# Optimization experiments

Hardware: AMD Instinct MI355X
Metric: run time of the kernel (lower is better)

Reference implementation:

```python
import jax, jax.numpy as jnp
import numpy as np

VOCAB = 40000
EMB = 128
INNER = 128
Q_LEN = 20


def setup_inputs() -> dict:
    key = jax.random.key(0)
    ks = jax.random.split(key, 16)
    B, S, NB = 32, 512, 20
    std = 0.1
    inp = {
        "memories": jax.random.normal(ks[0], (B, S, NB, EMB), jnp.float32),
        "stories": jax.random.normal(ks[1], (B, S, EMB), jnp.float32),
        "stories_mask": jnp.ones((B, S), jnp.float32),
        "queries": jax.random.randint(ks[2], (B, Q_LEN), 0, VOCAB, jnp.int32),
        "keys": jax.random.randint(ks[3], (NB,), 0, VOCAB, jnp.int32),
        # learned parameters
        "emb_table": jax.random.normal(ks[4], (VOCAB, EMB), jnp.float32) * std,
        "mult_mask": jnp.ones((Q_LEN, EMB), jnp.float32),
        "A": jax.random.normal(ks[5], (EMB, INNER), jnp.float32) * std,
        "Bm": jax.random.normal(ks[6], (EMB, INNER), jnp.float32) * std,
        "C": jax.random.normal(ks[7], (EMB, INNER), jnp.float32) * std,
        "v": jnp.ones((INNER,), jnp.float32),
        "D": jax.random.normal(ks[8], (EMB, INNER), jnp.float32) * std,
        "E": jax.random.normal(ks[9], (EMB, INNER), jnp.float32) * std,
        "F": jax.random.normal(ks[10], (EMB, INNER), jnp.float32) * std,
        "w": jnp.ones((INNER,), jnp.float32),
        "H": jax.random.normal(ks[11], (EMB, EMB), jnp.float32) * std,
        "R": jax.random.normal(ks[12], (EMB, VOCAB), jnp.float32) * std,
    }
    return inp


def reference(memories, stories, stories_mask, queries, keys,
              emb_table, mult_mask, A, Bm, C, v, D, E, F, w, H, R):
    # _reduce_query: embed tokens, apply positional multiplicative mask, sum over positions
    u = jnp.sum(emb_table[queries] * mult_mask, axis=1)            # [B, emb]

    # intratemporal (Bahdanau-style) attention over memory blocks
    ia = jnp.einsum('bsne,ei->bsni', memories, A)                  # [B,S,NB,inner]
    kb = emb_table[keys] @ Bm                                      # [NB,inner]
    qc = u @ C                                                     # [B,inner]
    intr_align = jnp.sum(v * jnp.tanh(ia + kb[None, None] + qc[:, None, None]), axis=3)  # [B,S,NB]
    intr_attn = jax.nn.softmax(intr_align, axis=2)[..., None]      # [B,S,NB,1]
    temporal_memory = jnp.sum(intr_attn * memories, axis=2)        # [B,S,emb]

    # temporal attention over story sentences (with sentence term E, softmax activation)
    td = temporal_memory @ D                                       # [B,S,inner]
    te = stories @ E                                               # [B,S,inner]
    tf = (u @ F)[:, None]                                          # [B,1,inner]
    temporal_align_unmasked = jnp.sum(w * jnp.tanh(td + te + tf), axis=2)  # [B,S]
    temporal_align = temporal_align_unmasked * stories_mask
    # softmax branch: additive -inf mask where stories_mask == 0 (inf*0 NaNs zeroed in torch)
    masked_logits = jnp.where(stories_mask != 0, temporal_align, -jnp.inf)
    temporal_attn = jax.nn.softmax(masked_logits, axis=1)          # [B,S]

    # output readout (standard memory-network head)
    o = jnp.sum(temporal_attn[..., None] * temporal_memory, axis=1)  # [B,emb]
    logits = (o + u @ H) @ R                                         # [B,vocab]
    return logits
```

## Files before the change

### kernel.cpp

```cpp
#include <hip/hip_runtime.h>
#include <hip/hip_bf16.h>

#define B_   32
#define S_   512
#define NB_  20
#define EMB_ 128
#define VOC_ 40000

typedef float f32x4 __attribute__((ext_vector_type(4)));
typedef _Float16 f16x8 __attribute__((ext_vector_type(8)));
typedef __fp16 fp16x2 __attribute__((ext_vector_type(2)));

union FragH { uint4 u; f16x8 h; };
union H2 { fp16x2 h; unsigned u; };

__device__ __forceinline__ unsigned pk2(float a, float b){
  H2 t; t.h = __builtin_amdgcn_cvt_pkrtz(a, b);
  return t.u;
}
__device__ __forceinline__ unsigned short f2h(float x){
  _Float16 h = (_Float16)x;
  return __builtin_bit_cast(unsigned short, h);
}
__device__ __forceinline__ float tanh_fast(float x){
  float e2 = __builtin_amdgcn_exp2f(x * 2.8853900817779268f);
  float r  = __builtin_amdgcn_rcpf(e2 + 1.f);
  return fmaf(-2.f, r, 1.f);
}


__global__ __launch_bounds__(128) void prep_kernel(
    const int* __restrict__ queries, const int* __restrict__ keys,
    const float* __restrict__ emb, const float* __restrict__ mmask,
    const float* __restrict__ A, const float* __restrict__ Bm,
    const float* __restrict__ C, const float* __restrict__ D,
    const float* __restrict__ E, const float* __restrict__ F,
    const float* __restrict__ H,
    float* __restrict__ tf_w, float* __restrict__ uh_w,
    float* __restrict__ kbq_w,
    unsigned short* __restrict__ afrag, unsigned short* __restrict__ w2frag)
{
  int bid = blockIdx.x, tid = threadIdx.x;
  if (bid < 32) {
    __shared__ float ulds[128];
    int b = bid;
    float s = 0.f;
    for (int q=0;q<NB_;q++){
      int tok = queries[b*NB_+q];
      s += emb[tok*128+tid]*mmask[q*128+tid];
    }
    ulds[tid] = s;
    __syncthreads();
    float sf=0.f, sh=0.f;
    for (int e=0;e<128;e++){
      float uv = ulds[e];
      sf += uv*F[e*128+tid];
      sh += uv*H[e*128+tid];
    }
    tf_w[b*128+tid]=sf; uh_w[b*128+tid]=sh;
  } else if (bid < 672) {
    __shared__ float ulds[128];
    __shared__ float ek[128];
    int idx = bid-32;
    int b = idx/20, n = idx - b*20;
    float s = 0.f;
    for (int q=0;q<NB_;q++){
      int tok = queries[b*NB_+q];
      s += emb[tok*128+tid]*mmask[q*128+tid];
    }
    ulds[tid] = s;
    ek[tid] = emb[keys[n]*128+tid];
    __syncthreads();
    float acc = 0.f;
    for (int e=0;e<128;e++){
      acc += ulds[e]*C[e*128+tid] + ek[e]*Bm[e*128+tid];
    }
    kbq_w[idx*128+tid] = acc;
  } else if (bid < 680) {
    int a = bid-672;
    for (int cc=0;cc<2;cc++){
      int c = (a*128+tid)*2+cc;
      int lane = c&63, kc = (c>>6)&3, nt = c>>8;
      int n2 = nt*16 + (lane&15);
      int k0 = kc*32 + (lane>>4)*8;
      alignas(16) unsigned short t[8];
      #pragma unroll
      for (int j=0;j<8;j++) t[j] = f2h(A[(k0+j)*128+n2]);
      *(uint4*)(afrag + c*8) = *(const uint4*)t;
    }
  } else {
    int wb = bid-680;
    for (int cc=0;cc<2;cc++){
      int c = (wb*128+tid)*2+cc;
      int lane = c&63, kc = (c>>6)&7, nt = c>>9;
      int n2 = nt*16 + (lane&15);
      int k0 = kc*32 + (lane>>4)*8;
      alignas(16) unsigned short t[8];
      #pragma unroll
      for (int j=0;j<8;j++){
        int k = k0+j;
        float x = (k<128) ? D[k*128+n2] : E[(k-128)*128+n2];
        t[j] = f2h(x);
      }
      *(uint4*)(w2frag + c*8) = *(const uint4*)t;
    }
  }
}

__global__ __launch_bounds__(256) void k2_kernel(
    const float* __restrict__ mem, const unsigned short* __restrict__ afrag,
    const float* __restrict__ kbq_w, const float* __restrict__ vvec,
    const float* __restrict__ stories, const unsigned short* __restrict__ w2frag,
    const float* __restrict__ tf_w, const float* __restrict__ wvec,
    const float* __restrict__ smask,
    unsigned short* __restrict__ tm_h, float* __restrict__ talign_w)
{
  __shared__ unsigned short mfr[5*4*64*8];
  __shared__ float alignP[4*80];
  __shared__ float attns[80];
  __shared__ float partial2[16];

  int g = blockIdx.x, tid = threadIdx.x;
  int b = g >> 7;

  int w = tid>>6, lane = tid&63;
  int lo16 = lane & 15, hi16 = lane >> 4;
  int p2 = w, e0 = (tid&63)*2;

  float2 sto = *(const float2*)(stories + ((size_t)(g*4+p2))*128 + e0);

  {
    int kq = (tid&31)*4;
    int kgs = kq>>5, s2s = (kq>>3)&3, offs = kq&7;
    int r0 = tid>>5;
    int cbs = s2s ^ ((kgs&1)<<2);
    int slot_e = (s2s<<4) | ((r0 ^ cbs) & 15);
    int slot_o = (s2s<<4) | (((r0^8) ^ cbs) & 15);
    unsigned addr_e = (unsigned)((kgs*64 + slot_e)*16 + offs*2);
    unsigned addr_o = (unsigned)((kgs*64 + slot_o)*16 + offs*2);
    const float4* gm = (const float4*)(mem) + (size_t)g*2560 + tid;
    #pragma unroll
    for (int mt=0; mt<5; ++mt){
      float4 d0 = gm[(2*mt)*256];
      float4 d1 = gm[(2*mt+1)*256];
      *(uint2*)((char*)mfr + addr_e + mt*4096) = make_uint2(pk2(d0.x,d0.y), pk2(d0.z,d0.w));
      *(uint2*)((char*)mfr + addr_o + mt*4096) = make_uint2(pk2(d1.x,d1.y), pk2(d1.z,d1.w));
    }
  }
  __syncthreads();

  int i0 = w*32 + lo16, i1 = i0 + 16;
  float vv0 = vvec[i0],       vv1 = vvec[i1];
  float tf0 = tf_w[b*128+i0], tf1 = tf_w[b*128+i1];
  float wv0 = wvec[i0],       wv1 = wvec[i1];
  const float* kbq0 = kbq_w + b*(NB_*128) + i0;

  f32x4 acc[5][2];
  #pragma unroll
  for (int mt=0;mt<5;mt++){ acc[mt][0]=(f32x4)(0.f); acc[mt][1]=(f32x4)(0.f); }
  #pragma unroll
  for (int kc=0;kc<4;kc++){
    FragH b0, b1;
    b0.u = *(const uint4*)(afrag + ((size_t)((2*w)*4+kc)*64 + lane)*8);
    b1.u = *(const uint4*)(afrag + ((size_t)((2*w+1)*4+kc)*64 + lane)*8);
    int slot = (hi16<<4) | ((lo16 ^ hi16 ^ ((kc&1)<<2)) & 15);
    #pragma unroll
    for (int mt=0;mt<5;mt++){
      FragH a;
      a.u = *(const uint4*)(mfr + ((mt*4+kc)*64 + slot)*8);
      acc[mt][0] = __builtin_amdgcn_mfma_f32_16x16x32_f16(a.h, b0.h, acc[mt][0], 0,0,0);
      acc[mt][1] = __builtin_amdgcn_mfma_f32_16x16x32_f16(a.h, b1.h, acc[mt][1], 0,0,0);
    }
  }

  #pragma unroll
  for (int mt=0;mt<5;mt++){
    #pragma unroll
    for (int r=0;r<4;r++){
      unsigned row = mt*16 + hi16*4 + r;
      unsigned p = row/20u;
      unsigned n = row - p*20u;
      float z0 = acc[mt][0][r] + kbq0[n*128];
      float z1 = acc[mt][1][r] + kbq0[n*128+16];
      float part = vv0*tanh_fast(z0) + vv1*tanh_fast(z1);
      part += __shfl_xor(part, 1);
      part += __shfl_xor(part, 2);
      part += __shfl_xor(part, 4);
      part += __shfl_xor(part, 8);
      if (lo16 == 0) alignP[w*80+row] = part;
    }
  }
  __syncthreads();

  {
    float av = -1e30f;
    if (lane < 20){
      int idx = w*20 + lane;
      av = alignP[idx] + alignP[80+idx] + alignP[160+idx] + alignP[240+idx];
    }
    float mx = av;
    #pragma unroll
    for (int d=1; d<64; d<<=1) mx = fmaxf(mx, __shfl_xor(mx, d));
    float ev = (lane<20) ? __expf(av - mx) : 0.f;
    float sm = ev;
    #pragma unroll
    for (int d=1; d<64; d<<=1) sm += __shfl_xor(sm, d);
    if (lane<20) attns[w*20+lane] = ev * __builtin_amdgcn_rcpf(sm);
  }

  unsigned otm;
  {
    int kg = e0>>5, s2 = (e0>>3)&3;
    int cb = s2 ^ ((kg&1)<<2);
    unsigned base = (unsigned)((kg*64 + (s2<<4))*16 + (e0&7)*2);
    float2 o = make_float2(0.f,0.f);
    #define TM_STEP(ROW) { \
      H2 q; q.u = *(const unsigned*)((const char*)mfr + base + (((ROW)>>4)*4096) + ((((ROW)&15) ^ cb) & 15)*16); \
      float a = attns[(ROW)]; \
      o.x += a*(float)q.h[0]; \
      o.y += a*(float)q.h[1]; }
    #define TM_20(P) { \
      TM_STEP((P)*20+0)  TM_STEP((P)*20+1)  TM_STEP((P)*20+2)  TM_STEP((P)*20+3)  \
      TM_STEP((P)*20+4)  TM_STEP((P)*20+5)  TM_STEP((P)*20+6)  TM_STEP((P)*20+7)  \
      TM_STEP((P)*20+8)  TM_STEP((P)*20+9)  TM_STEP((P)*20+10) TM_STEP((P)*20+11) \
      TM_STEP((P)*20+12) TM_STEP((P)*20+13) TM_STEP((P)*20+14) TM_STEP((P)*20+15) \
      TM_STEP((P)*20+16) TM_STEP((P)*20+17) TM_STEP((P)*20+18) TM_STEP((P)*20+19) }
    switch(p2){
      case 0: TM_20(0) break;
      case 1: TM_20(1) break;
      case 2: TM_20(2) break;
      default: TM_20(3) break;
    }
    #undef TM_20
    #undef TM_STEP
    otm = pk2(o.x, o.y);
    *(unsigned*)(tm_h + ((size_t)g*4+p2)*128 + e0) = otm;
  }
  __syncthreads();

  {
    int kcA = e0>>5;
    int lane2 = (((e0>>3)&3)<<4) | p2;
    *(unsigned*)(mfr + (kcA*64+lane2)*8 + (e0&7)) = otm;
    *(unsigned*)(mfr + ((kcA+4)*64+lane2)*8 + (e0&7)) = pk2(sto.x, sto.y);
  }
  __syncthreads();

  {
    f32x4 acc0 = (f32x4)(0.f), acc1 = (f32x4)(0.f);
    #pragma unroll
    for (int kc=0;kc<8;kc++){
      FragH af, b0, b1;
      af.u = *(const uint4*)(mfr + (kc*64+lane)*8);
      b0.u = *(const uint4*)(w2frag + ((size_t)((2*w)*8+kc)*64+lane)*8);
      b1.u = *(const uint4*)(w2frag + ((size_t)((2*w+1)*8+kc)*64+lane)*8);
      acc0 = __builtin_amdgcn_mfma_f32_16x16x32_f16(af.h, b0.h, acc0, 0,0,0);
      acc1 = __builtin_amdgcn_mfma_f32_16x16x32_f16(af.h, b1.h, acc1, 0,0,0);
    }
    if (hi16 == 0){
      #pragma unroll
      for (int r=0;r<4;r++){
        float part = wv0*tanh_fast(acc0[r] + tf0) + wv1*tanh_fast(acc1[r] + tf1);
        part += __shfl_xor(part,1);
        part += __shfl_xor(part,2);
        part += __shfl_xor(part,4);
        part += __shfl_xor(part,8);
        if (lo16==0) partial2[w*4+r] = part;
      }
    }
  }
  __syncthreads();

  if (tid < 4){
    float ta = partial2[tid]+partial2[4+tid]+partial2[8+tid]+partial2[12+tid];
    int flat = g*4+tid;
    float m = smask[flat];
    talign_w[flat] = (m != 0.0f) ? ta*m : -INFINITY;
  }
}

__global__ __launch_bounds__(256) void k3_kernel(
    const float* __restrict__ talign_w, const unsigned short* __restrict__ tm_h,
    const float* __restrict__ uh_w, float* __restrict__ ov_w)
{
  __shared__ float attn[512];
  __shared__ float red[256];
  __shared__ float2 red2[256];
  int bid = blockIdx.x, tid = threadIdx.x;
  int b = bid >> 3, ec = bid & 7;

  float v0 = talign_w[b*512+tid];
  float v1 = talign_w[b*512+256+tid];
  red[tid] = fmaxf(v0,v1);
  __syncthreads();
  for (int s=128;s>0;s>>=1){ if (tid<s) red[tid]=fmaxf(red[tid],red[tid+s]); __syncthreads(); }
  float M = red[0];
  __syncthreads();
  float e0v = __expf(v0-M), e1v = __expf(v1-M);
  red[tid] = e0v+e1v;
  __syncthreads();
  for (int s=128;s>0;s>>=1){ if (tid<s) red[tid]+=red[tid+s]; __syncthreads(); }
  float invZ = 1.f/red[0];
  attn[tid] = e0v*invZ;
  attn[256+tid] = e1v*invZ;
  __syncthreads();

  int e = ec*16 + (tid&7)*2;
  int sg = tid>>3;
  const unsigned short* tmb = tm_h + ((size_t)b*512 + sg*16)*128 + e;
  float2 a2 = make_float2(0.f,0.f);
  #pragma unroll 8
  for (int i=0;i<16;i++){
    H2 q; q.u = *(const unsigned*)(tmb + (size_t)i*128);
    float at = attn[sg*16+i];
    a2.x += at*(float)q.h[0];
    a2.y += at*(float)q.h[1];
  }
  red2[tid] = a2;
  __syncthreads();
  for (int s=128;s>=8;s>>=1){
    if (tid<s){ red2[tid].x += red2[tid+s].x; red2[tid].y += red2[tid+s].y; }
    __syncthreads();
  }
  if (tid<8){
    int e2 = ec*16 + tid*2;
    ov_w[b*128+e2]   = red2[tid].x + uh_w[b*128+e2];
    ov_w[b*128+e2+1] = red2[tid].y + uh_w[b*128+e2+1];
  }
}

__global__ __launch_bounds__(256) void k4_kernel(
    const float* __restrict__ ov_w, const float* __restrict__ R,
    float* __restrict__ out)
{
  int tid = threadIdx.x;
  int j = blockIdx.x*128 + (tid&63)*2;
  if (j >= VOC_) return;
  int bh = tid>>6;
  const float* ovb = ov_w + bh*8*128;
  float2 acc[8];
  #pragma unroll
  for (int bb=0;bb<8;bb++) acc[bb]=make_float2(0.f,0.f);
  for (int e=0;e<128;e+=4){
    float2 r0 = *(const float2*)(&R[(size_t)(e+0)*VOC_ + j]);
    float2 r1 = *(const float2*)(&R[(size_t)(e+1)*VOC_ + j]);
    float2 r2 = *(const float2*)(&R[(size_t)(e+2)*VOC_ + j]);
    float2 r3 = *(const float2*)(&R[(size_t)(e+3)*VOC_ + j]);
    #pragma unroll
    for (int bb=0;bb<8;bb++){
      float4 o = *(const float4*)(&ovb[bb*128+e]);
      acc[bb].x += o.x*r0.x + o.y*r1.x + o.z*r2.x + o.w*r3.x;
      acc[bb].y += o.x*r0.y + o.y*r1.y + o.z*r2.y + o.w*r3.y;
    }
  }
  #pragma unroll
  for (int bb=0;bb<8;bb++)
    *(float2*)(&out[(size_t)(bh*8+bb)*VOC_ + j]) = acc[bb];
}

extern "C" void kernel_launch(void* const* d_in, const int* in_sizes, int n_in,
                              void* d_out, int out_size, void* d_ws, size_t ws_size,
                              hipStream_t stream)
{
  const float* mem    = (const float*)d_in[0];
  const float* stories= (const float*)d_in[1];
  const float* smask  = (const float*)d_in[2];
  const int*   queries= (const int*)d_in[3];
  const int*   keys   = (const int*)d_in[4];
  const float* emb    = (const float*)d_in[5];
  const float* mmask  = (const float*)d_in[6];
  const float* A      = (const float*)d_in[7];
  const float* Bm     = (const float*)d_in[8];
  const float* C      = (const float*)d_in[9];
  const float* vvec   = (const float*)d_in[10];
  const float* D      = (const float*)d_in[11];
  const float* E      = (const float*)d_in[12];
  const float* F      = (const float*)d_in[13];
  const float* wvec   = (const float*)d_in[14];
  const float* H      = (const float*)d_in[15];
  const float* R      = (const float*)d_in[16];
  float* out = (float*)d_out;

  char* ws = (char*)d_ws;
  float* tf_w             = (float*)(ws + 0);
  float* uh_w             = (float*)(ws + 16384);
  float* kbq_w            = (float*)(ws + 32768);
  unsigned short* afrag   = (unsigned short*)(ws + 360448);
  unsigned short* w2frag  = (unsigned short*)(ws + 393216);
  unsigned short* tm_h    = (unsigned short*)(ws + 458752);
  float* talign_w         = (float*)(ws + 4653056);
  float* ov_w             = (float*)(ws + 4718592);

  prep_kernel<<<696,128,0,stream>>>(queries, keys, emb, mmask, A, Bm, C, D, E, F, H,
                                    tf_w, uh_w, kbq_w, afrag, w2frag);
  k2_kernel<<<4096,256,0,stream>>>(mem, afrag, kbq_w, vvec,
                                   stories, w2frag, tf_w, wvec, smask,
                                   tm_h, talign_w);
  k3_kernel<<<256,256,0,stream>>>(talign_w, tm_h, uh_w, ov_w);
  k4_kernel<<<313,256,0,stream>>>(ov_w, R, out);
}
```

Measured before the change: 370.7 us.

## Halve story positions per k2 block and double the grid

The intratemporal/temporal kernel now handles 2 story positions per 256-thread block instead of 4, and the launch grid doubles to 8192 blocks. Shared-memory staging shrinks to 3 MFMA row tiles, which should let more blocks be resident and spread the memory loads across more workgroups. In exchange, 8 of the 48 MFMA rows are padding, half the threads sit idle in the weighted-sum and store phases, and per-block fixed costs (weight fragment loads, barriers) are paid twice as often.

```diff
diff --git a/kernel.cpp b/kernel.cpp
--- a/kernel.cpp
+++ b/kernel.cpp
@@ -115,19 +115,21 @@
     const float* __restrict__ smask,
     unsigned short* __restrict__ tm_h, float* __restrict__ talign_w)
 {
-  __shared__ unsigned short mfr[5*4*64*8];
-  __shared__ float alignP[4*80];
-  __shared__ float attns[80];
-  __shared__ float partial2[16];
+  __shared__ unsigned short mfr[3*4*64*8];
+  __shared__ float alignP[4*40];
+  __shared__ float attns[40];
+  __shared__ float partial2[8];
 
   int g = blockIdx.x, tid = threadIdx.x;
-  int b = g >> 7;
+  int b = g >> 8;
 
   int w = tid>>6, lane = tid&63;
   int lo16 = lane & 15, hi16 = lane >> 4;
-  int p2 = w, e0 = (tid&63)*2;
-
-  float2 sto = *(const float2*)(stories + ((size_t)(g*4+p2))*128 + e0);
+
+  float2 sto = make_float2(0.f,0.f);
+  int p2s = (tid>>6)&1, e0s = (tid&63)*2;
+  if (tid >= 128)
+    sto = *(const float2*)(stories + ((size_t)(g*2+p2s))*128 + e0s);
 
   {
     int kq = (tid&31)*4;
@@ -138,14 +140,17 @@
     int slot_o = (s2s<<4) | (((r0^8) ^ cbs) & 15);
     unsigned addr_e = (unsigned)((kgs*64 + slot_e)*16 + offs*2);
     unsigned addr_o = (unsigned)((kgs*64 + slot_o)*16 + offs*2);
-    const float4* gm = (const float4*)(mem) + (size_t)g*2560 + tid;
-    #pragma unroll
-    for (int mt=0; mt<5; ++mt){
-      float4 d0 = gm[(2*mt)*256];
-      float4 d1 = gm[(2*mt+1)*256];
-      *(uint2*)((char*)mfr + addr_e + mt*4096) = make_uint2(pk2(d0.x,d0.y), pk2(d0.z,d0.w));
-      *(uint2*)((char*)mfr + addr_o + mt*4096) = make_uint2(pk2(d1.x,d1.y), pk2(d1.z,d1.w));
-    }
+    const float4* gm = (const float4*)(mem) + (size_t)g*1280 + tid;
+    float4 d0 = gm[0];
+    float4 d1 = gm[256];
+    float4 d2 = gm[512];
+    float4 d3 = gm[768];
+    float4 d4 = gm[1024];
+    *(uint2*)((char*)mfr + addr_e)        = make_uint2(pk2(d0.x,d0.y), pk2(d0.z,d0.w));
+    *(uint2*)((char*)mfr + addr_o)        = make_uint2(pk2(d1.x,d1.y), pk2(d1.z,d1.w));
+    *(uint2*)((char*)mfr + addr_e + 4096) = make_uint2(pk2(d2.x,d2.y), pk2(d2.z,d2.w));
+    *(uint2*)((char*)mfr + addr_o + 4096) = make_uint2(pk2(d3.x,d3.y), pk2(d3.z,d3.w));
+    *(uint2*)((char*)mfr + addr_e + 8192) = make_uint2(pk2(d4.x,d4.y), pk2(d4.z,d4.w));
   }
   __syncthreads();
 
@@ -155,9 +160,9 @@
   float wv0 = wvec[i0],       wv1 = wvec[i1];
   const float* kbq0 = kbq_w + b*(NB_*128) + i0;
 
-  f32x4 acc[5][2];
+  f32x4 acc[3][2];
   #pragma unroll
-  for (int mt=0;mt<5;mt++){ acc[mt][0]=(f32x4)(0.f); acc[mt][1]=(f32x4)(0.f); }
+  for (int mt=0;mt<3;mt++){ acc[mt][0]=(f32x4)(0.f); acc[mt][1]=(f32x4)(0.f); }
   #pragma unroll
   for (int kc=0;kc<4;kc++){
     FragH b0, b1;
@@ -165,7 +170,7 @@
     b1.u = *(const uint4*)(afrag + ((size_t)((2*w+1)*4+kc)*64 + lane)*8);
     int slot = (hi16<<4) | ((lo16 ^ hi16 ^ ((kc&1)<<2)) & 15);
     #pragma unroll
-    for (int mt=0;mt<5;mt++){
+    for (int mt=0;mt<3;mt++){
       FragH a;
       a.u = *(const uint4*)(mfr + ((mt*4+kc)*64 + slot)*8);
       acc[mt][0] = __builtin_amdgcn_mfma_f32_16x16x32_f16(a.h, b0.h, acc[mt][0], 0,0,0);
@@ -174,29 +179,31 @@
   }
 
   #pragma unroll
-  for (int mt=0;mt<5;mt++){
+  for (int mt=0;mt<3;mt++){
     #pragma unroll
     for (int r=0;r<4;r++){
       unsigned row = mt*16 + hi16*4 + r;
-      unsigned p = row/20u;
-      unsigned n = row - p*20u;
-      float z0 = acc[mt][0][r] + kbq0[n*128];
-      float z1 = acc[mt][1][r] + kbq0[n*128+16];
-      float part = vv0*tanh_fast(z0) + vv1*tanh_fast(z1);
-      part += __shfl_xor(part, 1);
-      part += __shfl_xor(part, 2);
-      part += __shfl_xor(part, 4);
-      part += __shfl_xor(part, 8);
-      if (lo16 == 0) alignP[w*80+row] = part;
-    }
-  }
-  __syncthreads();
-
-  {
+      if (row < 40){
+        unsigned p = row/20u;
+        unsigned n = row - p*20u;
+        float z0 = acc[mt][0][r] + kbq0[n*128];
+        float z1 = acc[mt][1][r] + kbq0[n*128+16];
+        float part = vv0*tanh_fast(z0) + vv1*tanh_fast(z1);
+        part += __shfl_xor(part, 1);
+        part += __shfl_xor(part, 2);
+        part += __shfl_xor(part, 4);
+        part += __shfl_xor(part, 8);
+        if (lo16 == 0) alignP[w*40+row] = part;
+      }
+    }
+  }
+  __syncthreads();
+
+  if (w < 2){
     float av = -1e30f;
     if (lane < 20){
       int idx = w*20 + lane;
-      av = alignP[idx] + alignP[80+idx] + alignP[160+idx] + alignP[240+idx];
+      av = alignP[idx] + alignP[40+idx] + alignP[80+idx] + alignP[120+idx];
     }
     float mx = av;
     #pragma unroll
@@ -208,11 +215,12 @@
     if (lane<20) attns[w*20+lane] = ev * __builtin_amdgcn_rcpf(sm);
   }
 
-  unsigned otm;
-  {
-    int kg = e0>>5, s2 = (e0>>3)&3;
+  unsigned otm = 0;
+  int p2t = tid>>6, e0t = (tid&63)*2;
+  if (tid < 128){
+    int kg = e0t>>5, s2 = (e0t>>3)&3;
     int cb = s2 ^ ((kg&1)<<2);
-    unsigned base = (unsigned)((kg*64 + (s2<<4))*16 + (e0&7)*2);
+    unsigned base = (unsigned)((kg*64 + (s2<<4))*16 + (e0t&7)*2);
     float2 o = make_float2(0.f,0.f);
     #define TM_STEP(ROW) { \
       H2 q; q.u = *(const unsigned*)((const char*)mfr + base + (((ROW)>>4)*4096) + ((((ROW)&15) ^ cb) & 15)*16); \
@@ -225,24 +233,22 @@
       TM_STEP((P)*20+8)  TM_STEP((P)*20+9)  TM_STEP((P)*20+10) TM_STEP((P)*20+11) \
       TM_STEP((P)*20+12) TM_STEP((P)*20+13) TM_STEP((P)*20+14) TM_STEP((P)*20+15) \
       TM_STEP((P)*20+16) TM_STEP((P)*20+17) TM_STEP((P)*20+18) TM_STEP((P)*20+19) }
-    switch(p2){
-      case 0: TM_20(0) break;
-      case 1: TM_20(1) break;
-      case 2: TM_20(2) break;
-      default: TM_20(3) break;
-    }
+    if (p2t == 0){ TM_20(0) } else { TM_20(1) }
     #undef TM_20
     #undef TM_STEP
     otm = pk2(o.x, o.y);
-    *(unsigned*)(tm_h + ((size_t)g*4+p2)*128 + e0) = otm;
-  }
-  __syncthreads();
-
-  {
-    int kcA = e0>>5;
-    int lane2 = (((e0>>3)&3)<<4) | p2;
-    *(unsigned*)(mfr + (kcA*64+lane2)*8 + (e0&7)) = otm;
-    *(unsigned*)(mfr + ((kcA+4)*64+lane2)*8 + (e0&7)) = pk2(sto.x, sto.y);
+    *(unsigned*)(tm_h + ((size_t)g*2+p2t)*128 + e0t) = otm;
+  }
+  __syncthreads();
+
+  if (tid < 128){
+    int kcA = e0t>>5;
+    int lane2 = (((e0t>>3)&3)<<4) | p2t;
+    *(unsigned*)(mfr + (kcA*64+lane2)*8 + (e0t&7)) = otm;
+  } else {
+    int kcA = 4 + (e0s>>5);
+    int lane2 = (((e0s>>3)&3)<<4) | p2s;
+    *(unsigned*)(mfr + (kcA*64+lane2)*8 + (e0s&7)) = pk2(sto.x, sto.y);
   }
   __syncthreads();
 
@@ -259,21 +265,21 @@
     }
     if (hi16 == 0){
       #pragma unroll
-      for (int r=0;r<4;r++){
+      for (int r=0;r<2;r++){
         float part = wv0*tanh_fast(acc0[r] + tf0) + wv1*tanh_fast(acc1[r] + tf1);
         part += __shfl_xor(part,1);
         part += __shfl_xor(part,2);
         part += __shfl_xor(part,4);
         part += __shfl_xor(part,8);
-        if (lo16==0) partial2[w*4+r] = part;
+        if (lo16==0) partial2[w*2+r] = part;
       }
     }
   }
   __syncthreads();
 
-  if (tid < 4){
-    float ta = partial2[tid]+partial2[4+tid]+partial2[8+tid]+partial2[12+tid];
-    int flat = g*4+tid;
+  if (tid < 2){
+    float ta = partial2[tid]+partial2[2+tid]+partial2[4+tid]+partial2[6+tid];
+    int flat = g*2+tid;
     float m = smask[flat];
     talign_w[flat] = (m != 0.0f) ? ta*m : -INFINITY;
   }
@@ -393,7 +399,7 @@
 
   prep_kernel<<<696,128,0,stream>>>(queries, keys, emb, mmask, A, Bm, C, D, E, F, H,
                                     tf_w, uh_w, kbq_w, afrag, w2frag);
-  k2_kernel<<<4096,256,0,stream>>>(mem, afrag, kbq_w, vvec,
+  k2_kernel<<<8192,256,0,stream>>>(mem, afrag, kbq_w, vvec,
                                    stories, w2frag, tf_w, wvec, smask,
                                    tm_h, talign_w);
   k3_kernel<<<256,256,0,stream>>>(talign_w, tm_h, uh_w, ov_w);
```

Result: slower. 379.6 us (+2.4%).
